# Kernel tuning notes

Measured on AMD Instinct MI355X. Metric: run time of the kernel, lower is better.

Reference implementation:

```python
import jax, jax.numpy as jnp
import numpy as np

N_TAU = 100  # steps per delay: dt = tau / N_TAU (backward code uses dt = 0.01*tau)


def F_model(x, y, t, W1, W2, b):
    # F(x(t), x(t - tau), t); t enters the signature but this Model is autonomous,
    # matching the repo's example models.
    return jnp.tanh(W1 @ x + W2 @ y + b)


def setup_inputs() -> dict:
    key = jax.random.key(0)
    d = 512
    k1, k2, k3, k4 = jax.random.split(key, 4)
    scale = 1.0 / np.sqrt(d).astype(np.float32)
    x_0 = jax.random.normal(k1, (d,), dtype=jnp.float32)
    W1 = jax.random.normal(k2, (d, d), dtype=jnp.float32) * scale
    W2 = jax.random.normal(k3, (d, d), dtype=jnp.float32) * scale
    b = jax.random.normal(k4, (d,), dtype=jnp.float32)
    tau = jnp.ones((), dtype=jnp.float32)  # time delay; dt = 0.01 * tau
    N = 2000  # = floor(T / dt) with T = 20, tau = 1
    return {"x_0": x_0, "tau": tau, "W1": W1, "W2": W2, "b": b, "N": N}


def reference(x_0, tau, W1, W2, b, N):
    """Forward-Euler DDE solve of x'(t) = F(x(t), x(t - tau), t), x(t) = x_0 for t <= 0.
    Returns the trajectory as a [d, N+1] array (kth column = state at step k),
    matching DDE_Solver's x_Trajectory layout."""
    d = x_0.shape[0]
    M = N_TAU + 1  # ring buffer holds the last N_tau+1 states
    dt = 0.01 * tau

    buf0 = jnp.zeros((d, M), dtype=x_0.dtype).at[:, 0].set(x_0)

    def step(buf, j):
        x_j = buf[:, j % M]
        # delayed state x(t_j - tau) = x_{j - N_tau}; (j - N_tau) % M == (j + 1) % M
        y_hist = buf[:, (j + 1) % M]
        y_j = jnp.where(j >= N_TAU, y_hist, x_0)  # pre-history: x(t) = x_0
        t_j = j * dt
        x_jp1 = x_j + dt * F_model(x_j, y_j, t_j, W1, W2, b)
        buf = buf.at[:, (j + 1) % M].set(x_jp1)
        return buf, x_jp1

    _, ys = jax.lax.scan(step, buf0, jnp.arange(N))  # ys: [N, d]
    return jnp.concatenate([x_0[:, None], ys.T], axis=1)  # [d, N+1]
```

## Files before the change

### kernel.cpp

```cpp
#include <hip/hip_runtime.h>


#define D     512
#define NTAU  100
#define M     112
#define HSLOT 101
#define NW    64

typedef unsigned long long u64;

__device__ __forceinline__ float lo_f(u64 v){ union{unsigned u; float f;} c; c.u=(unsigned)v; return c.f; }
__device__ __forceinline__ u64 pack_rec(unsigned tag, float x){ union{unsigned u; float f;} c; c.f=x; return ((u64)tag<<32)|(u64)c.u; }
__device__ __forceinline__ u64 ag_ld(const u64* p){
    return __hip_atomic_load(p, __ATOMIC_RELAXED, __HIP_MEMORY_SCOPE_AGENT);
}
__device__ __forceinline__ void ag_st(u64* p, u64 v){
    __hip_atomic_store(p, v, __ATOMIC_RELAXED, __HIP_MEMORY_SCOPE_AGENT);
}
__device__ __forceinline__ void iss8(const u64* p, u64 r[8]){
    #pragma unroll
    for (int i = 0; i < 8; ++i) r[i] = ag_ld(p + 64 * i);
}
__device__ __forceinline__ bool chk8(const u64 r[8], unsigned t){
    bool ok = true;
    #pragma unroll
    for (int i = 0; i < 8; ++i) ok &= ((unsigned)(r[i] >> 32) == t);
    return __all(ok);
}
__device__ __forceinline__ float sel8(const float* a, int k){
    float s = a[0];
    s = (k == 1) ? a[1] : s;  s = (k == 2) ? a[2] : s;
    s = (k == 3) ? a[3] : s;  s = (k == 4) ? a[4] : s;
    s = (k == 5) ? a[5] : s;  s = (k == 6) ? a[6] : s;
    s = (k == 7) ? a[7] : s;
    return s;
}

__global__ __launch_bounds__(64)
__attribute__((amdgpu_waves_per_eu(1, 1)))
void ndde_r8(
    const float* __restrict__ x0p, const float* __restrict__ taup,
    const float* __restrict__ W1,  const float* __restrict__ W2,
    const float* __restrict__ bb,  const int* __restrict__ Np,
    float* __restrict__ out, u64* __restrict__ ring,
    float* __restrict__ hist, int use_hist, float one)
{
    const int lane    = threadIdx.x & 63;
    const int wb      = blockIdx.x;
    const int rowbase = wb * 8;
    const int N       = Np[0];
    const float dt    = 0.01f * taup[0];

    float w1v[8][8], w2v[8][8];
    #pragma unroll
    for (int r = 0; r < 8; ++r){
        const float* p1 = W1 + (size_t)(rowbase + r) * D + lane;
        const float* p2 = W2 + (size_t)(rowbase + r) * D + lane;
        #pragma unroll
        for (int i = 0; i < 8; ++i){
            w1v[r][i] = p1[64 * i] * one;
            w2v[r][i] = p2[64 * i] * one;
        }
    }
    #pragma unroll
    for (int r = 0; r < 8; ++r){
        #pragma unroll
        for (int i = 0; i < 8; ++i)
            asm volatile("" : "+v"(w1v[r][i]), "+v"(w2v[r][i]));
    }

    float xv0[8];
    #pragma unroll
    for (int i = 0; i < 8; ++i) xv0[i] = x0p[64 * i + lane];
    float yp[8], a[8];
    #pragma unroll
    for (int r = 0; r < 8; ++r){
        float sy = 0.f, st = 0.f;
        #pragma unroll
        for (int i = 0; i < 8; ++i){
            sy = fmaf(w2v[r][i], xv0[i], sy);
            st = fmaf(w1v[r][i], xv0[i], st);
        }
        yp[r] = sy; a[r] = st + sy;
    }

    const int sel = lane & 7;
    #pragma unroll
    for (int r = 0; r < 8; ++r){
        a[r] += __shfl_xor(a[r], 1, 64);
        a[r] += __shfl_xor(a[r], 2, 64);
        a[r] += __shfl_xor(a[r], 4, 64);
    }
    float d0 = sel8(a, sel);
    d0 += __shfl_xor(d0, 8, 64);
    d0 += __shfl_xor(d0, 16, 64);
    d0 += __shfl_xor(d0, 32, 64);

    float xloc = 0.f, bval = 0.f;
    if (lane < 8){
        const int row = rowbase + lane;
        xloc = x0p[row];
        bval = bb[row];
        out[(size_t)row * (N + 1)] = xloc;
        if (N >= 1){
            const float x1 = xloc + dt * tanhf(d0 + bval);
            xloc = x1;
            ag_st(ring + D + row, pack_rec(2u, x1));
            out[(size_t)row * (N + 1) + 1] = x1;
        }
    }

    float* myh = hist + (size_t)wb * HSLOT * D;

    u64 xa[8], xb[8];
    float xf[8];
    float obuf[16];
    #pragma unroll
    for (int k = 0; k < 16; ++k) obuf[k] = 0.f;
    int sx = 1, sp = 2, syr = 1;
    int hw = 0, hr = 0;
    bool dead = false;

    for (int j = 1; j < N && !dead; ++j){
        const bool needy  = (j > NTAU);
        const unsigned tx = (unsigned)(j + 1);
        const u64* px = ring + (size_t)sx * D + lane;

        u64 yr[8];
        if (!use_hist && needy){
            const u64* py = ring + (size_t)syr * D + lane;
            iss8(py, yr);
        }

        iss8(px, xa);
        int it = 0;
        for (;;){
            iss8(px, xb);
            if (chk8(xa, tx)) break;
            iss8(px, xa);
            if (chk8(xb, tx)){
                #pragma unroll
                for (int i = 0; i < 8; ++i) xa[i] = xb[i];
                break;
            }
            if ((it += 2) > (1 << 21)){ dead = true; break; }
        }
        #pragma unroll
        for (int i = 0; i < 8; ++i) xf[i] = lo_f(xa[i]);

        if (!use_hist && needy){
            const unsigned ty = (unsigned)(j - NTAU + 1);
            if (!chk8(yr, ty)){
                const u64* py = ring + (size_t)syr * D + lane;
                int it2 = 0;
                for (;;){
                    iss8(py, yr);
                    if (chk8(yr, ty)) break;
                    if (++it2 > (1 << 21)){ dead = true; break; }
                }
            }
            #pragma unroll
            for (int r = 0; r < 8; ++r){
                float sy = 0.f;
                #pragma unroll
                for (int i = 0; i < 8; ++i) sy = fmaf(w2v[r][i], lo_f(yr[i]), sy);
                yp[r] = sy;
            }
        }

        #pragma unroll
        for (int r = 0; r < 8; ++r){
            float s = yp[r];
            #pragma unroll
            for (int i = 0; i < 8; ++i) s = fmaf(w1v[r][i], xf[i], s);
            a[r] = s;
        }
        #pragma unroll
        for (int r = 0; r < 8; ++r){
            a[r] += __shfl_xor(a[r], 1, 64);
            a[r] += __shfl_xor(a[r], 2, 64);
            a[r] += __shfl_xor(a[r], 4, 64);
        }
        float dd = sel8(a, sel);
        dd += __shfl_xor(dd, 8, 64);
        dd += __shfl_xor(dd, 16, 64);
        dd += __shfl_xor(dd, 32, 64);

        if (lane < 8){
            const float xn = xloc + dt * tanhf(dd + bval);
            xloc = xn;
            const int row = rowbase + lane;
            ag_st(ring + (size_t)sp * D + row, pack_rec(tx + 1, xn));

            #pragma unroll
            for (int k = 0; k < 15; ++k) obuf[k] = obuf[k + 1];
            obuf[15] = xn;
            if (((j - 1) & 15) == 15){
                float* po = out + (size_t)row * (N + 1) + (j - 14);
                #pragma unroll
                for (int k = 0; k < 16; ++k) po[k] = obuf[k];
            }
        }

        if (use_hist){
            float* hwp = myh + (size_t)hw * D + lane;
            #pragma unroll
            for (int i = 0; i < 8; ++i) hwp[64 * i] = xf[i];
            if (j >= NTAU){
                const float* hrp = myh + (size_t)hr * D + lane;
                float yv[8];
                #pragma unroll
                for (int i = 0; i < 8; ++i) yv[i] = hrp[64 * i];
                #pragma unroll
                for (int r = 0; r < 8; ++r){
                    float sy = 0.f;
                    #pragma unroll
                    for (int i = 0; i < 8; ++i) sy = fmaf(w2v[r][i], yv[i], sy);
                    yp[r] = sy;
                }
                hr = (hr == HSLOT - 1) ? 0 : hr + 1;
            }
            hw = (hw == HSLOT - 1) ? 0 : hw + 1;
        }

        sx = (sx == M - 1) ? 0 : sx + 1;
        sp = (sp == M - 1) ? 0 : sp + 1;
        if (j >= NTAU + 1) syr = (syr == M - 1) ? 0 : syr + 1;
    }

    if (N >= 2 && lane < 8){
        const int cnt = ((N - 2) & 15) + 1;
        const int row = rowbase + lane;
        float* po = out + (size_t)row * (N + 1);
        #pragma unroll
        for (int k = 0; k < 16; ++k){
            if (k >= 16 - cnt) po[N - 15 + k] = obuf[k];
        }
    }
}

extern "C" void kernel_launch(void* const* d_in, const int* in_sizes, int n_in,
                              void* d_out, int out_size, void* d_ws, size_t ws_size,
                              hipStream_t stream)
{
    const float* x0  = (const float*)d_in[0];
    const float* tau = (const float*)d_in[1];
    const float* W1  = (const float*)d_in[2];
    const float* W2  = (const float*)d_in[3];
    const float* b   = (const float*)d_in[4];
    const int*   Np  = (const int*)  d_in[5];

    const size_t ring_bytes = (size_t)M * D * 8;
    const size_t hist_bytes = (size_t)NW * HSLOT * D * 4;
    const int use_hist = (ws_size >= ring_bytes + hist_bytes) ? 1 : 0;

    u64*   ring = (u64*)d_ws;
    float* hist = (float*)((char*)d_ws + ring_bytes);
    const float one = 1.0f;

    hipLaunchKernelGGL(ndde_r8, dim3(NW), dim3(64), 0, stream,
                       x0, tau, W1, W2, b, Np, (float*)d_out, ring, hist, use_hist, one);
}
```

Measured before the change: 2.935 ms.

## Precompute delayed W2 products into LDS queue and prefetch next ring slot

Each step now computes W2·x_j right when x_j arrives and keeps the reduced per-row result in a small LDS queue indexed by the delay. This takes the delayed-state reload and its W2 matvec off the critical path, and it removes the global history buffer. The wave also skips polling for its own rows by substituting its local value, and it issues the next slot's loads before storing. The cost is an extra reduction per step done after the state is published, plus a more involved tag check.

```diff
diff --git a/kernel.cpp b/kernel.cpp
--- a/kernel.cpp
+++ b/kernel.cpp
@@ -1,11 +1,11 @@
 #include <hip/hip_runtime.h>
 
 
-#define D     512
-#define NTAU  100
-#define M     112
-#define HSLOT 101
-#define NW    64
+#define D    512
+#define NTAU 100
+#define M    112
+#define QD   101
+#define NW   64
 
 typedef unsigned long long u64;
 
@@ -21,10 +21,11 @@
     #pragma unroll
     for (int i = 0; i < 8; ++i) r[i] = ag_ld(p + 64 * i);
 }
-__device__ __forceinline__ bool chk8(const u64 r[8], unsigned t){
+__device__ __forceinline__ bool chk8m(const u64 r[8], unsigned t, int i0, bool ownm){
     bool ok = true;
     #pragma unroll
-    for (int i = 0; i < 8; ++i) ok &= ((unsigned)(r[i] >> 32) == t);
+    for (int i = 0; i < 8; ++i)
+        ok &= (((unsigned)(r[i] >> 32) == t) || (ownm && i == i0));
     return __all(ok);
 }
 __device__ __forceinline__ float sel8(const float* a, int k){
@@ -35,21 +36,39 @@
     s = (k == 7) ? a[7] : s;
     return s;
 }
+__device__ __forceinline__ float reduce8(float a[8], int sel){
+    #pragma unroll
+    for (int r = 0; r < 8; ++r){
+        a[r] += __shfl_xor(a[r], 1, 64);
+        a[r] += __shfl_xor(a[r], 2, 64);
+        a[r] += __shfl_xor(a[r], 4, 64);
+    }
+    float d = sel8(a, sel);
+    d += __shfl_xor(d, 8, 64);
+    d += __shfl_xor(d, 16, 64);
+    d += __shfl_xor(d, 32, 64);
+    return d;
+}
 
 __global__ __launch_bounds__(64)
 __attribute__((amdgpu_waves_per_eu(1, 1)))
-void ndde_r8(
+void ndde_r9(
     const float* __restrict__ x0p, const float* __restrict__ taup,
     const float* __restrict__ W1,  const float* __restrict__ W2,
     const float* __restrict__ bb,  const int* __restrict__ Np,
-    float* __restrict__ out, u64* __restrict__ ring,
-    float* __restrict__ hist, int use_hist, float one)
+    float* __restrict__ out, u64* __restrict__ ring, float one)
 {
+    __shared__ float qlds[QD * 8];
+
     const int lane    = threadIdx.x & 63;
     const int wb      = blockIdx.x;
     const int rowbase = wb * 8;
     const int N       = Np[0];
     const float dt    = 0.01f * taup[0];
+    const int sel     = lane & 7;
+    const int i0      = wb >> 3;
+    const int lb      = (wb * 8) & 63;
+    const bool ownm   = ((unsigned)(lane - lb)) < 8u;
 
     float w1v[8][8], w2v[8][8];
     #pragma unroll
@@ -72,29 +91,20 @@
     float xv0[8];
     #pragma unroll
     for (int i = 0; i < 8; ++i) xv0[i] = x0p[64 * i + lane];
-    float yp[8], a[8];
-    #pragma unroll
-    for (int r = 0; r < 8; ++r){
-        float sy = 0.f, st = 0.f;
+    float ax[8], ay[8];
+    #pragma unroll
+    for (int r = 0; r < 8; ++r){
+        float st = 0.f, sy = 0.f;
         #pragma unroll
         for (int i = 0; i < 8; ++i){
+            st = fmaf(w1v[r][i], xv0[i], st);
             sy = fmaf(w2v[r][i], xv0[i], sy);
-            st = fmaf(w1v[r][i], xv0[i], st);
-        }
-        yp[r] = sy; a[r] = st + sy;
-    }
-
-    const int sel = lane & 7;
-    #pragma unroll
-    for (int r = 0; r < 8; ++r){
-        a[r] += __shfl_xor(a[r], 1, 64);
-        a[r] += __shfl_xor(a[r], 2, 64);
-        a[r] += __shfl_xor(a[r], 4, 64);
-    }
-    float d0 = sel8(a, sel);
-    d0 += __shfl_xor(d0, 8, 64);
-    d0 += __shfl_xor(d0, 16, 64);
-    d0 += __shfl_xor(d0, 32, 64);
+        }
+        ax[r] = st; ay[r] = sy;
+    }
+    const float xdot0 = reduce8(ax, sel);
+    const float q0    = reduce8(ay, sel);
+    if (lane < 8) qlds[0 * 8 + lane] = q0;
 
     float xloc = 0.f, bval = 0.f;
     if (lane < 8){
@@ -103,135 +113,108 @@
         bval = bb[row];
         out[(size_t)row * (N + 1)] = xloc;
         if (N >= 1){
-            const float x1 = xloc + dt * tanhf(d0 + bval);
+            const float x1 = xloc + dt * tanhf(xdot0 + q0 + bval);
             xloc = x1;
             ag_st(ring + D + row, pack_rec(2u, x1));
             out[(size_t)row * (N + 1) + 1] = x1;
         }
     }
 
-    float* myh = hist + (size_t)wb * HSLOT * D;
-
-    u64 xa[8], xb[8];
-    float xf[8];
+    u64 cur[8];
+    iss8(ring + (size_t)1 * D + lane, cur);
+
     float obuf[16];
     #pragma unroll
     for (int k = 0; k < 16; ++k) obuf[k] = 0.f;
-    int sx = 1, sp = 2, syr = 1;
-    int hw = 0, hr = 0;
+
+    int sx = 1, sp = 2;
+    int qw = 1, qr = 0;
     bool dead = false;
 
     for (int j = 1; j < N && !dead; ++j){
-        const bool needy  = (j > NTAU);
         const unsigned tx = (unsigned)(j + 1);
         const u64* px = ring + (size_t)sx * D + lane;
 
-        u64 yr[8];
-        if (!use_hist && needy){
-            const u64* py = ring + (size_t)syr * D + lane;
-            iss8(py, yr);
-        }
-
-        iss8(px, xa);
-        int it = 0;
-        for (;;){
-            iss8(px, xb);
-            if (chk8(xa, tx)) break;
-            iss8(px, xa);
-            if (chk8(xb, tx)){
-                #pragma unroll
-                for (int i = 0; i < 8; ++i) xa[i] = xb[i];
-                break;
+        float ydot = 0.f;
+        if (lane < 8) ydot = qlds[qr * 8 + lane];
+
+        if (!chk8m(cur, tx, i0, ownm)){
+            u64 alt[8];
+            iss8(px, alt);
+            int it = 0;
+            for (;;){
+                iss8(px, cur);
+                if (chk8m(alt, tx, i0, ownm)){
+                    #pragma unroll
+                    for (int i = 0; i < 8; ++i) cur[i] = alt[i];
+                    break;
+                }
+                iss8(px, alt);
+                if (chk8m(cur, tx, i0, ownm)) break;
+                if ((it += 2) > (1 << 21)){ dead = true; break; }
             }
-            if ((it += 2) > (1 << 21)){ dead = true; break; }
-        }
-        #pragma unroll
-        for (int i = 0; i < 8; ++i) xf[i] = lo_f(xa[i]);
-
-        if (!use_hist && needy){
-            const unsigned ty = (unsigned)(j - NTAU + 1);
-            if (!chk8(yr, ty)){
-                const u64* py = ring + (size_t)syr * D + lane;
-                int it2 = 0;
-                for (;;){
-                    iss8(py, yr);
-                    if (chk8(yr, ty)) break;
-                    if (++it2 > (1 << 21)){ dead = true; break; }
-                }
-            }
-            #pragma unroll
-            for (int r = 0; r < 8; ++r){
-                float sy = 0.f;
-                #pragma unroll
-                for (int i = 0; i < 8; ++i) sy = fmaf(w2v[r][i], lo_f(yr[i]), sy);
-                yp[r] = sy;
-            }
-        }
-
+        }
+        float xf[8];
+        #pragma unroll
+        for (int i = 0; i < 8; ++i) xf[i] = lo_f(cur[i]);
+        {
+            const float xsub = __shfl(xloc, lane - lb, 64);
+            #pragma unroll
+            for (int i = 0; i < 8; ++i)
+                xf[i] = (ownm && i == i0) ? xsub : xf[i];
+        }
+
+        float a[8];
         #pragma unroll
         for (int r = 0; r < 8; ++r){
-            float s = yp[r];
+            float s = 0.f;
             #pragma unroll
             for (int i = 0; i < 8; ++i) s = fmaf(w1v[r][i], xf[i], s);
             a[r] = s;
         }
+        const float xdot = reduce8(a, sel);
+
+        float xn = 0.f;
+        if (lane < 8){
+            xn = xloc + dt * tanhf(xdot + ydot + bval);
+            xloc = xn;
+        }
+
+        iss8(ring + (size_t)sp * D + lane, cur);
+        if (lane < 8)
+            ag_st(ring + (size_t)sp * D + (rowbase + lane), pack_rec(tx + 1, xn));
+
+        float c[8];
         #pragma unroll
         for (int r = 0; r < 8; ++r){
-            a[r] += __shfl_xor(a[r], 1, 64);
-            a[r] += __shfl_xor(a[r], 2, 64);
-            a[r] += __shfl_xor(a[r], 4, 64);
-        }
-        float dd = sel8(a, sel);
-        dd += __shfl_xor(dd, 8, 64);
-        dd += __shfl_xor(dd, 16, 64);
-        dd += __shfl_xor(dd, 32, 64);
+            float s = 0.f;
+            #pragma unroll
+            for (int i = 0; i < 8; ++i) s = fmaf(w2v[r][i], xf[i], s);
+            c[r] = s;
+        }
+        const float qj = reduce8(c, sel);
+        if (lane < 8) qlds[qw * 8 + lane] = qj;
 
         if (lane < 8){
-            const float xn = xloc + dt * tanhf(dd + bval);
-            xloc = xn;
-            const int row = rowbase + lane;
-            ag_st(ring + (size_t)sp * D + row, pack_rec(tx + 1, xn));
-
             #pragma unroll
             for (int k = 0; k < 15; ++k) obuf[k] = obuf[k + 1];
             obuf[15] = xn;
             if (((j - 1) & 15) == 15){
-                float* po = out + (size_t)row * (N + 1) + (j - 14);
+                float* po = out + (size_t)(rowbase + lane) * (N + 1) + (j - 14);
                 #pragma unroll
                 for (int k = 0; k < 16; ++k) po[k] = obuf[k];
             }
         }
 
-        if (use_hist){
-            float* hwp = myh + (size_t)hw * D + lane;
-            #pragma unroll
-            for (int i = 0; i < 8; ++i) hwp[64 * i] = xf[i];
-            if (j >= NTAU){
-                const float* hrp = myh + (size_t)hr * D + lane;
-                float yv[8];
-                #pragma unroll
-                for (int i = 0; i < 8; ++i) yv[i] = hrp[64 * i];
-                #pragma unroll
-                for (int r = 0; r < 8; ++r){
-                    float sy = 0.f;
-                    #pragma unroll
-                    for (int i = 0; i < 8; ++i) sy = fmaf(w2v[r][i], yv[i], sy);
-                    yp[r] = sy;
-                }
-                hr = (hr == HSLOT - 1) ? 0 : hr + 1;
-            }
-            hw = (hw == HSLOT - 1) ? 0 : hw + 1;
-        }
-
-        sx = (sx == M - 1) ? 0 : sx + 1;
+        sx = sp;
         sp = (sp == M - 1) ? 0 : sp + 1;
-        if (j >= NTAU + 1) syr = (syr == M - 1) ? 0 : syr + 1;
+        qw = (qw == QD - 1) ? 0 : qw + 1;
+        if (j >= NTAU) qr = (qr == QD - 1) ? 0 : qr + 1;
     }
 
     if (N >= 2 && lane < 8){
         const int cnt = ((N - 2) & 15) + 1;
-        const int row = rowbase + lane;
-        float* po = out + (size_t)row * (N + 1);
+        float* po = out + (size_t)(rowbase + lane) * (N + 1);
         #pragma unroll
         for (int k = 0; k < 16; ++k){
             if (k >= 16 - cnt) po[N - 15 + k] = obuf[k];
@@ -250,14 +233,9 @@
     const float* b   = (const float*)d_in[4];
     const int*   Np  = (const int*)  d_in[5];
 
-    const size_t ring_bytes = (size_t)M * D * 8;
-    const size_t hist_bytes = (size_t)NW * HSLOT * D * 4;
-    const int use_hist = (ws_size >= ring_bytes + hist_bytes) ? 1 : 0;
-
-    u64*   ring = (u64*)d_ws;
-    float* hist = (float*)((char*)d_ws + ring_bytes);
+    u64* ring = (u64*)d_ws;
     const float one = 1.0f;
 
-    hipLaunchKernelGGL(ndde_r8, dim3(NW), dim3(64), 0, stream,
-                       x0, tau, W1, W2, b, Np, (float*)d_out, ring, hist, use_hist, one);
-}
+    hipLaunchKernelGGL(ndde_r9, dim3(NW), dim3(64), 0, stream,
+                       x0, tau, W1, W2, b, Np, (float*)d_out, ring, one);
+}
```

Result: slower. 3.314 ms (+12.9%).
